# Performance work log

Hardware: AMD Instinct MI355X
Metric: run time of the kernel (lower is better)

## Reference

```python
import jax, jax.numpy as jnp
import numpy as np
import math

L, C, H, W = 5, 256, 128, 384

def _subset_masks(L):
    # For each agent i, enumerate all non-empty subsets S of the other L-1 agents.
    # masks[i, s, :] is the indicator of S union {i}; wgt[i, s] = |S|!(L-|S|-1)!/L!.
    S = 2 ** (L - 1) - 1
    masks = np.zeros((L, S, L), dtype=np.float32)
    wgt = np.zeros((L, S), dtype=np.float32)
    for i in range(L):
        others = [j for j in range(L) if j != i]
        for m in range(1, 2 ** (L - 1)):
            bits = [others[k] for k in range(L - 1) if (m >> k) & 1]
            card = len(bits)
            masks[i, m - 1, bits] = 1.0
            masks[i, m - 1, i] = 1.0
            wgt[i, m - 1] = math.factorial(card) * math.factorial(L - card - 1) / math.factorial(L)
    return masks, wgt

_MASKS, _WGT = _subset_masks(L)

def setup_inputs() -> dict:
    key = jax.random.key(0)
    k1, k2, k3 = jax.random.split(key, 3)
    feats = jax.random.normal(k1, (L, C, H, W), dtype=jnp.float32)
    bound = 1.0 / np.sqrt(C)  # nn.Linear default init scale
    w = jax.random.uniform(k2, (C, 1), dtype=jnp.float32, minval=-bound, maxval=bound)
    b = jax.random.uniform(k3, (1,), dtype=jnp.float32, minval=-bound, maxval=bound)
    return {"feats": feats, "w": w, "b": b}

def reference(feats, w, b):
    Lc, Cc, Hc, Wc = feats.shape
    N = Hc * Wc
    x = feats.reshape(Lc, Cc, N).transpose(0, 2, 1)  # (L, N, C) == rearrange 'l c h w -> l (h w) c'
    # Linear is affine, so lin(sum_j f_j) = sum_j (f_j @ w) + b. Precompute per-agent projections.
    z = jnp.einsum('lnc,co->ln', x, w)  # (L, N), no bias yet
    masks = jnp.asarray(_MASKS)  # (L, S, L)
    wgt = jnp.asarray(_WGT)      # (L, S)
    # ReLU(lin(sum over subset S u {i})) for every agent / subset, vectorized
    subset_val = jax.nn.relu(jnp.einsum('lsm,mn->lsn', masks, z) + b[0])  # (L, S, N)
    self_val = jax.nn.relu(z + b[0])  # (L, N) = contrib_feats_i
    # shapley[i] = sum_S w(|S|) * (v(S u {i}) - v({i})) + v({i}) / L
    shap = (jnp.einsum('ls,lsn->ln', wgt, subset_val)
            - jnp.sum(wgt, axis=1)[:, None] * self_val
            + self_val / Lc)  # (L, N)
    wsoft = jax.nn.softmax(shap, axis=0)  # softmax over agents
    out = jnp.einsum('lnc,ln->nc', x, wsoft)  # (N, C)
    return out.T.reshape(Cc, Hc, Wc)
```

## Files before the change

kernel.cpp:

```cpp
#include <hip/hip_runtime.h>

#define L 5
#define C 256
#define HH 128
#define WW 384
#define N (HH * WW)

__global__ __launch_bounds__(256) void k_z(const float* __restrict__ feats,
                                           const float* __restrict__ w,
                                           float* __restrict__ z) {
    __shared__ float wl[C];
    const int tid = threadIdx.x;
    wl[tid] = w[tid];
    __syncthreads();

    const int BPL = N / 256;
    const int l = blockIdx.x / BPL;
    const int n = (blockIdx.x % BPL) * 256 + tid;

    const float* fp = feats + (size_t)l * C * N + n;
    float acc = 0.f;
#pragma unroll 8
    for (int c = 0; c < C; ++c) {
        acc += fp[(size_t)c * N] * wl[c];
    }
    z[l * N + n] = acc;
}

__global__ __launch_bounds__(256) void k_shap(const float* __restrict__ bptr,
                                              float* __restrict__ z) {
    const int n = blockIdx.x * 256 + threadIdx.x;
    const float bv = bptr[0];

    float zv[L];
#pragma unroll
    for (int l = 0; l < L; ++l) zv[l] = z[l * N + n];

    const float wc1 = 0.05f;
    const float wc2 = 1.f / 30.f;
    const float wc3 = 0.05f;
    const float wc4 = 0.2f;
    const float wcard[5] = {0.f, wc1, wc2, wc3, wc4};

    float shap[L];
#pragma unroll
    for (int i = 0; i < L; ++i) {
        int others[4];
        {
            int k = 0;
#pragma unroll
            for (int j = 0; j < L; ++j)
                if (j != i) others[k++] = j;
        }
        float acc = 0.f;
#pragma unroll
        for (int m = 1; m < 16; ++m) {
            float s = zv[i] + bv;
            int card = 0;
#pragma unroll
            for (int kk = 0; kk < 4; ++kk) {
                if ((m >> kk) & 1) { s += zv[others[kk]]; ++card; }
            }
            acc += wcard[card] * fmaxf(s, 0.f);
        }
        const float self = fmaxf(zv[i] + bv, 0.f);
        shap[i] = acc - 0.6f * self;
    }

    float mx = shap[0];
#pragma unroll
    for (int i = 1; i < L; ++i) mx = fmaxf(mx, shap[i]);
    float e[L];
    float sum = 0.f;
#pragma unroll
    for (int i = 0; i < L; ++i) { e[i] = __expf(shap[i] - mx); sum += e[i]; }
    const float inv = 1.f / sum;
#pragma unroll
    for (int i = 0; i < L; ++i) z[i * N + n] = e[i] * inv;
}

__global__ __launch_bounds__(256) void k_out(const float* __restrict__ feats,
                                             const float* __restrict__ wsoft,
                                             float* __restrict__ out) {
    const int tid = threadIdx.x;
    const int BPC = (N / 4) / 256;
    const int c = blockIdx.x / BPC;
    const int n = ((blockIdx.x % BPC) * 256 + tid) * 4;

    float4 acc = make_float4(0.f, 0.f, 0.f, 0.f);
#pragma unroll
    for (int l = 0; l < L; ++l) {
        const float4 f = *(const float4*)(feats + ((size_t)(l * C + c)) * N + n);
        const float4 s = *(const float4*)(wsoft + (size_t)l * N + n);
        acc.x += f.x * s.x;
        acc.y += f.y * s.y;
        acc.z += f.z * s.z;
        acc.w += f.w * s.w;
    }
    *(float4*)(out + (size_t)c * N + n) = acc;
}

extern "C" void kernel_launch(void* const* d_in, const int* in_sizes, int n_in,
                              void* d_out, int out_size, void* d_ws, size_t ws_size,
                              hipStream_t stream) {
    const float* feats = (const float*)d_in[0];
    const float* w     = (const float*)d_in[1];
    const float* bptr  = (const float*)d_in[2];
    float* out = (float*)d_out;
    float* z   = (float*)d_ws;

    k_z<<<L * (N / 256), 256, 0, stream>>>(feats, w, z);
    k_shap<<<N / 256, 256, 0, stream>>>(bptr, z);
    k_out<<<C * ((N / 4) / 256), 256, 0, stream>>>(feats, z, out);
}
```

Baseline: 396.0 us.

## Fuse projection, Shapley softmax and weighted sum into one LDS-tiled kernel

Replaces three kernels with one. Each block loads all L*C rows for 8 spatial positions into LDS once, computes the per-agent projections with wave shuffles and LDS atomics, runs the Shapley softmax for its 8 positions, then produces the output from the LDS tile. This cuts the feature tensor reads from two passes over HBM to one and drops the z workspace round trip. In exchange each block uses about 40KB of LDS and reads only 32-byte segments per row, which may limit occupancy and coalescing; block indices are swizzled to spread accesses.

```diff
diff --git a/kernel.cpp b/kernel.cpp
--- a/kernel.cpp
+++ b/kernel.cpp
@@ -5,99 +5,122 @@
 #define HH 128
 #define WW 384
 #define N (HH * WW)
+#define TN 8
+#define NBLK (N / TN)
+#define ROWS (L * C)
 
-__global__ __launch_bounds__(256) void k_z(const float* __restrict__ feats,
-                                           const float* __restrict__ w,
-                                           float* __restrict__ z) {
-    __shared__ float wl[C];
-    const int tid = threadIdx.x;
-    wl[tid] = w[tid];
+__global__ __launch_bounds__(256) void k_fused(const float* __restrict__ feats,
+                                               const float* __restrict__ w,
+                                               const float* __restrict__ bptr,
+                                               float* __restrict__ out) {
+    __shared__ float tile[ROWS * TN];
+    __shared__ float wlds[C];
+    __shared__ float zl[L][TN];
+    __shared__ float wsl[L][TN];
+
+    const int t = threadIdx.x;
+
+    const int blk = (blockIdx.x & 7) * (NBLK / 8) + (blockIdx.x >> 3);
+    const int n0 = blk * TN;
+
+    wlds[t] = w[t];
+    if (t < L * TN) ((float*)zl)[t] = 0.f;
     __syncthreads();
 
-    const int BPL = N / 256;
-    const int l = blockIdx.x / BPL;
-    const int n = (blockIdx.x % BPL) * 256 + tid;
+    const float bv = bptr[0];
+    const int n4 = t & 1;
+    const int r0 = t >> 1;
 
-    const float* fp = feats + (size_t)l * C * N + n;
-    float acc = 0.f;
-#pragma unroll 8
-    for (int c = 0; c < C; ++c) {
-        acc += fp[(size_t)c * N] * wl[c];
+    float za = 0.f, zb = 0.f, zc = 0.f, zd = 0.f;
+#pragma unroll
+    for (int k = 0; k < 10; ++k) {
+        const int r = r0 + 128 * k;
+        const int c = r & 255;
+        const float4 v = *(const float4*)(feats + (size_t)r * N + n0 + n4 * 4);
+        *(float4*)(&tile[(size_t)(t + 256 * k) * 4]) = v;
+        const float wc = wlds[c];
+        za += wc * v.x; zb += wc * v.y; zc += wc * v.z; zd += wc * v.w;
+        if (k & 1) {
+            float s0 = za, s1 = zb, s2 = zc, s3 = zd;
+#pragma unroll
+            for (int st = 2; st <= 32; st <<= 1) {
+                s0 += __shfl_xor(s0, st);
+                s1 += __shfl_xor(s1, st);
+                s2 += __shfl_xor(s2, st);
+                s3 += __shfl_xor(s3, st);
+            }
+            if ((t & 63) < 2) {
+                const int l = k >> 1;
+                const int nn = n4 * 4;
+                atomicAdd(&zl[l][nn + 0], s0);
+                atomicAdd(&zl[l][nn + 1], s1);
+                atomicAdd(&zl[l][nn + 2], s2);
+                atomicAdd(&zl[l][nn + 3], s3);
+            }
+            za = zb = zc = zd = 0.f;
+        }
     }
-    z[l * N + n] = acc;
-}
+    __syncthreads();
 
-__global__ __launch_bounds__(256) void k_shap(const float* __restrict__ bptr,
-                                              float* __restrict__ z) {
-    const int n = blockIdx.x * 256 + threadIdx.x;
-    const float bv = bptr[0];
+    if (t < TN) {
+        float zv[L];
+#pragma unroll
+        for (int l = 0; l < L; ++l) zv[l] = zl[l][t];
 
-    float zv[L];
+        const float wcard[5] = {0.f, 0.05f, 1.f / 30.f, 0.05f, 0.2f};
+        float shap[L];
 #pragma unroll
-    for (int l = 0; l < L; ++l) zv[l] = z[l * N + n];
-
-    const float wc1 = 0.05f;
-    const float wc2 = 1.f / 30.f;
-    const float wc3 = 0.05f;
-    const float wc4 = 0.2f;
-    const float wcard[5] = {0.f, wc1, wc2, wc3, wc4};
-
-    float shap[L];
-#pragma unroll
-    for (int i = 0; i < L; ++i) {
-        int others[4];
-        {
-            int k = 0;
+        for (int i = 0; i < L; ++i) {
+            int others[4];
+            int kk = 0;
 #pragma unroll
             for (int j = 0; j < L; ++j)
-                if (j != i) others[k++] = j;
+                if (j != i) others[kk++] = j;
+            float acc = 0.f;
+#pragma unroll
+            for (int m = 1; m < 16; ++m) {
+                float s = zv[i] + bv;
+                int card = 0;
+#pragma unroll
+                for (int q = 0; q < 4; ++q)
+                    if ((m >> q) & 1) { s += zv[others[q]]; ++card; }
+                acc += wcard[card] * fmaxf(s, 0.f);
+            }
+            const float self = fmaxf(zv[i] + bv, 0.f);
+            shap[i] = acc - 0.6f * self;
         }
-        float acc = 0.f;
+        float mx = shap[0];
 #pragma unroll
-        for (int m = 1; m < 16; ++m) {
-            float s = zv[i] + bv;
-            int card = 0;
+        for (int i = 1; i < L; ++i) mx = fmaxf(mx, shap[i]);
+        float e[L], sum = 0.f;
 #pragma unroll
-            for (int kk = 0; kk < 4; ++kk) {
-                if ((m >> kk) & 1) { s += zv[others[kk]]; ++card; }
-            }
-            acc += wcard[card] * fmaxf(s, 0.f);
+        for (int i = 0; i < L; ++i) { e[i] = __expf(shap[i] - mx); sum += e[i]; }
+        const float inv = 1.f / sum;
+#pragma unroll
+        for (int i = 0; i < L; ++i) wsl[i][t] = e[i] * inv;
+    }
+    __syncthreads();
+
+    float wr[L][4];
+#pragma unroll
+    for (int l = 0; l < L; ++l)
+#pragma unroll
+        for (int j = 0; j < 4; ++j) wr[l][j] = wsl[l][n4 * 4 + j];
+
+#pragma unroll
+    for (int k2 = 0; k2 < 2; ++k2) {
+        const int c = r0 + 128 * k2;
+        float4 acc = make_float4(0.f, 0.f, 0.f, 0.f);
+#pragma unroll
+        for (int l = 0; l < L; ++l) {
+            const float4 f = *(const float4*)(&tile[(size_t)(l * 512 + t + 256 * k2) * 4]);
+            acc.x += f.x * wr[l][0];
+            acc.y += f.y * wr[l][1];
+            acc.z += f.z * wr[l][2];
+            acc.w += f.w * wr[l][3];
         }
-        const float self = fmaxf(zv[i] + bv, 0.f);
-        shap[i] = acc - 0.6f * self;
+        *(float4*)(out + (size_t)c * N + n0 + n4 * 4) = acc;
     }
-
-    float mx = shap[0];
-#pragma unroll
-    for (int i = 1; i < L; ++i) mx = fmaxf(mx, shap[i]);
-    float e[L];
-    float sum = 0.f;
-#pragma unroll
-    for (int i = 0; i < L; ++i) { e[i] = __expf(shap[i] - mx); sum += e[i]; }
-    const float inv = 1.f / sum;
-#pragma unroll
-    for (int i = 0; i < L; ++i) z[i * N + n] = e[i] * inv;
-}
-
-__global__ __launch_bounds__(256) void k_out(const float* __restrict__ feats,
-                                             const float* __restrict__ wsoft,
-                                             float* __restrict__ out) {
-    const int tid = threadIdx.x;
-    const int BPC = (N / 4) / 256;
-    const int c = blockIdx.x / BPC;
-    const int n = ((blockIdx.x % BPC) * 256 + tid) * 4;
-
-    float4 acc = make_float4(0.f, 0.f, 0.f, 0.f);
-#pragma unroll
-    for (int l = 0; l < L; ++l) {
-        const float4 f = *(const float4*)(feats + ((size_t)(l * C + c)) * N + n);
-        const float4 s = *(const float4*)(wsoft + (size_t)l * N + n);
-        acc.x += f.x * s.x;
-        acc.y += f.y * s.y;
-        acc.z += f.z * s.z;
-        acc.w += f.w * s.w;
-    }
-    *(float4*)(out + (size_t)c * N + n) = acc;
 }
 
 extern "C" void kernel_launch(void* const* d_in, const int* in_sizes, int n_in,
@@ -107,9 +130,6 @@
     const float* w     = (const float*)d_in[1];
     const float* bptr  = (const float*)d_in[2];
     float* out = (float*)d_out;
-    float* z   = (float*)d_ws;
 
-    k_z<<<L * (N / 256), 256, 0, stream>>>(feats, w, z);
-    k_shap<<<N / 256, 256, 0, stream>>>(bptr, z);
-    k_out<<<C * ((N / 4) / 256), 256, 0, stream>>>(feats, z, out);
+    k_fused<<<NBLK, 256, 0, stream>>>(feats, w, bptr, out);
 }
```

Measured after the change: 371.2 us. 6.3% less time.
